# Kernel tuning notes

Measured on AMD Instinct MI355X. Metric: run time of the kernel, lower is better.

## Reference

```python
import jax, jax.numpy as jnp
import numpy as np
from jax import lax

B, C, D, H, W = 2, 128, 16, 16, 16
CH = C // 2
BN_EPS = 1e-5


def setup_inputs() -> dict:
    key = jax.random.key(0)
    ks = jax.random.split(key, 20)
    s = 0.02  # weight init scale
    inp = {
        "mri_feat": jax.random.normal(ks[0], (B, C, D, H, W), jnp.float32),
        "pet_feat": jax.random.normal(ks[1], (B, C, D, H, W), jnp.float32),
        # 1x1x1 conv projections stored as [out, in]
        "qw": jax.random.normal(ks[2], (C, C), jnp.float32) * s,
        "qb": jnp.zeros((C,), jnp.float32),
        "kw": jax.random.normal(ks[3], (C, C), jnp.float32) * s,
        "kb": jnp.zeros((C,), jnp.float32),
        "vw": jax.random.normal(ks[4], (C, C), jnp.float32) * s,
        "vb": jnp.zeros((C,), jnp.float32),
        # SE channel attention: C -> C/2 -> C
        "ca_w1": jax.random.normal(ks[5], (CH, C), jnp.float32) * s,
        "ca_b1": jnp.zeros((CH,), jnp.float32),
        "ca_w2": jax.random.normal(ks[6], (C, CH), jnp.float32) * s,
        "ca_b2": jnp.zeros((C,), jnp.float32),
        # conv1: 3x3x3 conv C -> C/2, then BN, then 1x1x1 conv C/2 -> C
        "c1_w": jax.random.normal(ks[7], (CH, C, 3, 3, 3), jnp.float32) * s,
        "c1_b": jnp.zeros((CH,), jnp.float32),
        "bn_gamma": jnp.ones((CH,), jnp.float32),
        "bn_beta": jnp.zeros((CH,), jnp.float32),
        "bn_mean": jnp.zeros((CH,), jnp.float32),
        "bn_var": jnp.ones((CH,), jnp.float32),
        "c2_w": jax.random.normal(ks[8], (C, CH), jnp.float32) * s,
        "c2_b": jnp.zeros((C,), jnp.float32),
    }
    return inp


def _conv1x1(x, w, b):
    # pointwise 3D conv == channel matmul
    return jnp.einsum('bcdhw,oc->bodhw', x, w) + b[None, :, None, None, None]


def reference(mri_feat, pet_feat, qw, qb, kw, kb, vw, vb,
              ca_w1, ca_b1, ca_w2, ca_b2,
              c1_w, c1_b, bn_gamma, bn_beta, bn_mean, bn_var,
              c2_w, c2_b):
    # --- SE channel attention on mri+pet ---
    pooled = jnp.mean(mri_feat + pet_feat, axis=(2, 3, 4))            # [B, C]
    t = jax.nn.relu(jnp.einsum('bc,oc->bo', pooled, ca_w1) + ca_b1)   # [B, C/2]
    cw = jax.nn.sigmoid(jnp.einsum('bh,oh->bo', t, ca_w2) + ca_b2)    # [B, C]
    cw = cw[:, :, None, None, None]
    mri_w = mri_feat * cw
    pet_w = pet_feat * cw

    # --- QKV (1x1x1 convs) ---
    Q = _conv1x1(mri_w, qw, qb)
    K = _conv1x1(pet_w, kw, kb)
    V = _conv1x1(pet_w, vw, vb)

    # --- full spatial cross attention ---
    scores = jnp.einsum('bcdhw,bcDHW->bdhwDHW', Q, K)   # [B,D,H,W,D,H,W]
    # NOTE: faithful to torch: softmax over LAST axis only (key W axis)
    attn = jax.nn.softmax(scores, axis=-1)
    fused = jnp.einsum('bdhwDHW,bcDHW->bcdhw', attn, V)

    # --- conv1 block: Conv3x3 -> ReLU -> BN(eval) -> Conv1x1 ---
    x = fused + mri_w
    y = lax.conv_general_dilated(
        x, c1_w, window_strides=(1, 1, 1), padding=((1, 1), (1, 1), (1, 1)),
        dimension_numbers=('NCDHW', 'OIDHW', 'NCDHW'))
    y = y + c1_b[None, :, None, None, None]
    y = jax.nn.relu(y)
    inv = lax.rsqrt(bn_var + BN_EPS)
    y = (y - bn_mean[None, :, None, None, None]) * (bn_gamma * inv)[None, :, None, None, None] \
        + bn_beta[None, :, None, None, None]
    out = _conv1x1(y, c2_w, c2_b)
    return out
```

## Files before the change

kernel.cpp:

```cpp
#include <hip/hip_runtime.h>
#include <hip/hip_bf16.h>
#include <math.h>

#define BB 2
#define CC 128
#define CHH 64
#define DD 16
#define NN 4096
#define SP 256
#define KTOT 3456
#define NKS 8

typedef float  f32x4 __attribute__((ext_vector_type(4)));
typedef short  s16x4 __attribute__((ext_vector_type(4)));
typedef short  s16x8 __attribute__((ext_vector_type(8)));

static __device__ __forceinline__ unsigned short f2bf(float x) {
    __hip_bfloat16 h = __float2bfloat16(x);
    return __builtin_bit_cast(unsigned short, h);
}

__global__ __launch_bounds__(256) void k_prep(const float* __restrict__ c1w, const float* __restrict__ c2w,
                                              const float* __restrict__ bg, const float* __restrict__ bbeta,
                                              const float* __restrict__ bm, const float* __restrict__ bv,
                                              const float* __restrict__ c2b,
                                              const float* __restrict__ qw, const float* __restrict__ kw,
                                              const float* __restrict__ vw,
                                              unsigned short* __restrict__ Wb,
                                              unsigned short* __restrict__ w2p,
                                              float* __restrict__ b2p,
                                              unsigned short* __restrict__ qwb,
                                              unsigned short* __restrict__ kwb,
                                              unsigned short* __restrict__ vwb) {
    int idx = blockIdx.x * 256 + threadIdx.x;
    for (int e = idx; e < CHH * KTOT; e += gridDim.x * 256) {
        int h = e / KTOT, rem = e % KTOT, tap = rem >> 7, c = rem & 127;
        Wb[e] = f2bf(c1w[(h * CC + c) * 27 + tap]);
    }
    for (int e = idx; e < CC * CC; e += gridDim.x * 256) {
        qwb[e] = f2bf(qw[e]);
        kwb[e] = f2bf(kw[e]);
        vwb[e] = f2bf(vw[e]);
    }
    for (int e = idx; e < CC * CHH; e += gridDim.x * 256) {
        int h = e & 63;
        float iv = rsqrtf(bv[h] + 1e-5f);
        w2p[e] = f2bf(c2w[e] * bg[h] * iv);
    }
    if (idx < CC) {
        float s = c2b[idx];
        for (int h = 0; h < CHH; h++) {
            float iv = rsqrtf(bv[h] + 1e-5f);
            s += c2w[idx * CHH + h] * (bbeta[h] - bm[h] * bg[h] * iv);
        }
        b2p[idx] = s;
    }
}

__global__ __launch_bounds__(256) void k_pool(const float* __restrict__ mri,
                                              const float* __restrict__ pet,
                                              float* __restrict__ pooled) {
    int bc = blockIdx.x;
    const float* m = mri + (size_t)bc * NN;
    const float* p = pet + (size_t)bc * NN;
    float s = 0.f;
    for (int i = threadIdx.x; i < NN; i += 256) s += m[i] + p[i];
    __shared__ float red[256];
    red[threadIdx.x] = s;
    __syncthreads();
    for (int off = 128; off > 0; off >>= 1) {
        if (threadIdx.x < off) red[threadIdx.x] += red[threadIdx.x + off];
        __syncthreads();
    }
    if (threadIdx.x == 0) pooled[bc] = red[0] * (1.0f / NN);
}

__global__ __launch_bounds__(128) void k_cw(const float* __restrict__ pooled,
                                            const float* __restrict__ w1, const float* __restrict__ b1,
                                            const float* __restrict__ w2, const float* __restrict__ b2,
                                            float* __restrict__ cw) {
    __shared__ float pl[BB * CC];
    __shared__ float tl[BB * CHH];
    int t = threadIdx.x;
    pl[t] = pooled[t];
    pl[t + 128] = pooled[t + 128];
    __syncthreads();
    {
        int b = t >> 6, h = t & 63;
        float acc = b1[h];
        for (int c = 0; c < CC; c++) acc += pl[b * CC + c] * w1[h * CC + c];
        tl[b * CHH + h] = fmaxf(acc, 0.f);
    }
    __syncthreads();
    for (int b = 0; b < BB; b++) {
        float acc = b2[t];
        for (int h = 0; h < CHH; h++) acc += tl[b * CHH + h] * w2[t * CHH + h];
        cw[b * CC + t] = 1.f / (1.f + __expf(-acc));
    }
}

__global__ __launch_bounds__(256) void k_qkv(const float* __restrict__ mri, const float* __restrict__ pet,
                                             const float* __restrict__ cw,
                                             const unsigned short* __restrict__ qwb, const float* __restrict__ qb,
                                             const unsigned short* __restrict__ kwb, const float* __restrict__ kb,
                                             const unsigned short* __restrict__ vwb, const float* __restrict__ vb,
                                             unsigned short* __restrict__ Qt, unsigned short* __restrict__ Kt,
                                             unsigned short* __restrict__ Vc) {
    __shared__ unsigned short am[32][136];
    __shared__ unsigned short ap[32][136];
    int blk = blockIdx.x;
    int b = blk >> 7;
    int n0 = (blk & 127) * 32;
    int t = threadIdx.x;
    for (int e = t; e < 64 * 32; e += 256) {
        int c2 = (e >> 5) << 1, j = e & 31;
        float cw0 = cw[b * CC + c2], cw1 = cw[b * CC + c2 + 1];
        size_t g0 = (size_t)(b * CC + c2) * NN + n0 + j;
        unsigned int pm = (unsigned int)f2bf(mri[g0] * cw0) | ((unsigned int)f2bf(mri[g0 + NN] * cw1) << 16);
        unsigned int pp = (unsigned int)f2bf(pet[g0] * cw0) | ((unsigned int)f2bf(pet[g0 + NN] * cw1) << 16);
        *(unsigned int*)&am[j][c2] = pm;
        *(unsigned int*)&ap[j][c2] = pp;
    }
    __syncthreads();
    int wv = t >> 6, lane = t & 63;
    int lrow = lane & 15, lg = lane >> 4;
    int o0 = wv * 32;

    s16x8 bf[2][4];
    s16x8 wf[2][4];
    f32x4 acc[2][2];

#define QKV_MAT(WPTR, BIAS, ACT)                                                            \
    {                                                                                       \
        _Pragma("unroll")                                                                   \
        for (int nt = 0; nt < 2; nt++)                                                      \
            _Pragma("unroll")                                                               \
            for (int ks = 0; ks < 4; ks++)                                                  \
                bf[nt][ks] = *(const s16x8*)&ACT[nt * 16 + lrow][ks * 32 + lg * 8];         \
        _Pragma("unroll")                                                                   \
        for (int m = 0; m < 2; m++)                                                         \
            _Pragma("unroll")                                                               \
            for (int ks = 0; ks < 4; ks++)                                                  \
                wf[m][ks] = *(const s16x8*)&WPTR[(size_t)(o0 + m * 16 + lrow) * CC + ks * 32 + lg * 8]; \
        _Pragma("unroll")                                                                   \
        for (int m = 0; m < 2; m++) {                                                       \
            float b0 = BIAS[o0 + m * 16 + lg * 4 + 0];                                      \
            float b1 = BIAS[o0 + m * 16 + lg * 4 + 1];                                      \
            float b2v = BIAS[o0 + m * 16 + lg * 4 + 2];                                     \
            float b3 = BIAS[o0 + m * 16 + lg * 4 + 3];                                      \
            _Pragma("unroll")                                                               \
            for (int nt = 0; nt < 2; nt++) {                                                \
                acc[m][nt] = (f32x4){b0, b1, b2v, b3};                                      \
                _Pragma("unroll")                                                           \
                for (int ks = 0; ks < 4; ks++)                                              \
                    acc[m][nt] = __builtin_amdgcn_mfma_f32_16x16x32_bf16(wf[m][ks], bf[nt][ks], acc[m][nt], 0, 0, 0); \
            }                                                                               \
        }                                                                                   \
    }

    QKV_MAT(qwb, qb, am);
#pragma unroll
    for (int m = 0; m < 2; m++)
#pragma unroll
        for (int nt = 0; nt < 2; nt++) {
            s16x4 q4;
#pragma unroll
            for (int r = 0; r < 4; r++) q4[r] = (short)f2bf(acc[m][nt][r]);
            *(s16x4*)&Qt[((size_t)b * NN + n0 + nt * 16 + lrow) * CC + o0 + m * 16 + lg * 4] = q4;
        }
    QKV_MAT(kwb, kb, ap);
#pragma unroll
    for (int m = 0; m < 2; m++)
#pragma unroll
        for (int nt = 0; nt < 2; nt++) {
            s16x4 k4;
#pragma unroll
            for (int r = 0; r < 4; r++) k4[r] = (short)f2bf(acc[m][nt][r]);
            *(s16x4*)&Kt[((size_t)b * NN + n0 + nt * 16 + lrow) * CC + o0 + m * 16 + lg * 4] = k4;
        }
    QKV_MAT(vwb, vb, ap);
#pragma unroll
    for (int m = 0; m < 2; m++)
#pragma unroll
        for (int nt = 0; nt < 2; nt++)
#pragma unroll
            for (int r = 0; r < 4; r++)
                Vc[((size_t)b * CC + o0 + m * 16 + lg * 4 + r) * NN + n0 + nt * 16 + lrow] =
                    (unsigned short)f2bf(acc[m][nt][r]);
#undef QKV_MAT
}

#define QW 32
__global__ __launch_bounds__(512) void k_attn(const unsigned short* __restrict__ Qt,
                                              const unsigned short* __restrict__ Kt,
                                              const unsigned short* __restrict__ Vc,
                                              float* __restrict__ Opart) {
    __shared__ unsigned short Ks[2][32][136];
    __shared__ unsigned short Vs[2][128][40];
    int bid = blockIdx.x;
    int ks = bid & 7;
    int r = bid >> 3;
    int qc = r >> 1;
    int b = r & 1;
    int t = threadIdx.x;
    int wv = t >> 6;
    int lane = t & 63;
    int lrow = lane & 15;
    int lg = lane >> 4;
    int q0 = qc * 256 + wv * 32;

    const unsigned short* Qb = Qt + (size_t)b * NN * CC;
    const unsigned short* Kb = Kt + (size_t)b * NN * CC;
    const unsigned short* Vb = Vc + (size_t)b * CC * NN;

    int sj = t >> 4, sseg = t & 15;
    int svc = t >> 2, svg = t & 3;

#define STAGE(BUF, K0)                                                                     \
    {                                                                                      \
        *(s16x8*)&Ks[BUF][sj][sseg * 8] = *(const s16x8*)(Kb + (size_t)((K0) + sj) * CC + sseg * 8); \
        *(s16x8*)&Vs[BUF][svc][svg * 8] = *(const s16x8*)(Vb + (size_t)svc * NN + (K0) + svg * 8);   \
    }

    s16x8 qf[2][4];
#pragma unroll
    for (int qt = 0; qt < 2; qt++)
#pragma unroll
        for (int cc = 0; cc < 4; cc++)
            qf[qt][cc] = *(const s16x8*)(Qb + (size_t)(q0 + qt * 16 + lrow) * CC + cc * 32 + lg * 8);

    f32x4 acc[2][8];
#pragma unroll
    for (int qt = 0; qt < 2; qt++)
#pragma unroll
        for (int ct = 0; ct < 8; ct++) acc[qt][ct] = (f32x4){0.f, 0.f, 0.f, 0.f};

    int kbase = ks * 512;
    STAGE(0, kbase);
#pragma unroll 1
    for (int i = 0; i < 16; i++) {
        __syncthreads();
        if (i + 1 < 16) STAGE((i + 1) & 1, kbase + (i + 1) * 32);
        int cur = i & 1;
        f32x4 sc[2][2];
#pragma unroll
        for (int kt = 0; kt < 2; kt++) {
            s16x8 kf[4];
#pragma unroll
            for (int cc = 0; cc < 4; cc++)
                kf[cc] = *(const s16x8*)&Ks[cur][kt * 16 + lrow][cc * 32 + lg * 8];
#pragma unroll
            for (int qt = 0; qt < 2; qt++) {
                f32x4 a = (f32x4){0.f, 0.f, 0.f, 0.f};
#pragma unroll
                for (int cc = 0; cc < 4; cc++)
                    a = __builtin_amdgcn_mfma_f32_16x16x32_bf16(kf[cc], qf[qt][cc], a, 0, 0, 0);
                sc[qt][kt] = a;
            }
        }
        s16x8 pf[2];
#pragma unroll
        for (int qt = 0; qt < 2; qt++) {
#pragma unroll
            for (int kt = 0; kt < 2; kt++) {
                f32x4 s = sc[qt][kt];
                float m = fmaxf(fmaxf(s[0], s[1]), fmaxf(s[2], s[3]));
                m = fmaxf(m, __shfl_xor(m, 16));
                m = fmaxf(m, __shfl_xor(m, 32));
                float e0 = __expf(s[0] - m), e1 = __expf(s[1] - m);
                float e2 = __expf(s[2] - m), e3 = __expf(s[3] - m);
                float sum = e0 + e1 + e2 + e3;
                sum += __shfl_xor(sum, 16);
                sum += __shfl_xor(sum, 32);
                float inv = 1.0f / sum;
                pf[qt][kt * 4 + 0] = (short)f2bf(e0 * inv);
                pf[qt][kt * 4 + 1] = (short)f2bf(e1 * inv);
                pf[qt][kt * 4 + 2] = (short)f2bf(e2 * inv);
                pf[qt][kt * 4 + 3] = (short)f2bf(e3 * inv);
            }
        }
#pragma unroll
        for (int ct = 0; ct < 8; ct++) {
            s16x4 v0 = *(const s16x4*)&Vs[cur][ct * 16 + lrow][4 * lg];
            s16x4 v1 = *(const s16x4*)&Vs[cur][ct * 16 + lrow][16 + 4 * lg];
            s16x8 vf = (s16x8){v0[0], v0[1], v0[2], v0[3], v1[0], v1[1], v1[2], v1[3]};
            acc[0][ct] = __builtin_amdgcn_mfma_f32_16x16x32_bf16(vf, pf[0], acc[0][ct], 0, 0, 0);
            acc[1][ct] = __builtin_amdgcn_mfma_f32_16x16x32_bf16(vf, pf[1], acc[1][ct], 0, 0, 0);
        }
    }
#undef STAGE
    float* Op = Opart + ((size_t)(ks * BB + b) * NN) * CC;
#pragma unroll
    for (int qt = 0; qt < 2; qt++)
#pragma unroll
        for (int ct = 0; ct < 8; ct++)
            *(f32x4*)&Op[(size_t)(q0 + qt * 16 + lrow) * CC + ct * 16 + lg * 4] = acc[qt][ct];
}

__global__ __launch_bounds__(256) void k_comb(const float* __restrict__ Opart,
                                              const float* __restrict__ mri, const float* __restrict__ cw,
                                              unsigned short* __restrict__ Xb) {
    __shared__ float tl[128][33];
    __shared__ float cws[128];
    int bid = blockIdx.x;
    int b = bid >> 7, n0 = (bid & 127) * 32;
    int t = threadIdx.x;
    if (t < 128) cws[t] = cw[b * CC + t];
    {
        int c = t >> 1, half = t & 1;
        const float* src = mri + (size_t)(b * CC + c) * NN + n0 + half * 16;
#pragma unroll
        for (int j = 0; j < 4; j++) {
            f32x4 v = *(const f32x4*)(src + j * 4);
            tl[c][half * 16 + j * 4 + 0] = v[0];
            tl[c][half * 16 + j * 4 + 1] = v[1];
            tl[c][half * 16 + j * 4 + 2] = v[2];
            tl[c][half * 16 + j * 4 + 3] = v[3];
        }
    }
    __syncthreads();
    {
        int n = t >> 3, c0 = (t & 7) * 16;
        size_t rowoff = (size_t)(n0 + n) * CC + c0;
        s16x8 o0v, o1v;
#pragma unroll
        for (int ci = 0; ci < 4; ci++) {
            f32x4 s = (f32x4){0.f, 0.f, 0.f, 0.f};
#pragma unroll
            for (int ks = 0; ks < NKS; ks++) {
                f32x4 p = *(const f32x4*)&Opart[((size_t)(ks * BB + b) * NN) * CC + rowoff + ci * 4];
                s[0] += p[0]; s[1] += p[1]; s[2] += p[2]; s[3] += p[3];
            }
#pragma unroll
            for (int j = 0; j < 4; j++) {
                int c = c0 + ci * 4 + j;
                float v = s[j] + tl[c][n] * cws[c];
                if (ci < 2) o0v[ci * 4 + j] = (short)f2bf(v);
                else        o1v[(ci - 2) * 4 + j] = (short)f2bf(v);
            }
        }
        unsigned short* dst = Xb + ((size_t)b * NN + n0 + n) * CC + c0;
        *(s16x8*)dst = o0v;
        *(s16x8*)(dst + 8) = o1v;
    }
}

__global__ __launch_bounds__(512) void k_attn_fb(const unsigned short* __restrict__ Qt,
                                                 const unsigned short* __restrict__ Kt,
                                                 const unsigned short* __restrict__ Vc,
                                                 const float* __restrict__ mri, const float* __restrict__ cw,
                                                 unsigned short* __restrict__ Xb) {
    __shared__ float Op[8][16][68];
    int bid = blockIdx.x;
    int lid = (bid & 7) * 32 + (bid >> 3);
    int b = lid >> 7;
    int q0 = (lid & 127) * QW;
    int t = threadIdx.x;
    int wv = t >> 6;
    int lane = t & 63;
    int lrow = lane & 15;
    int lg = lane >> 4;

    const unsigned short* Qb = Qt + (size_t)b * NN * CC;
    const unsigned short* Kb = Kt + (size_t)b * NN * CC;
    const unsigned short* Vb = Vc + (size_t)b * CC * NN;

    s16x8 qf[2][4];
#pragma unroll
    for (int qt = 0; qt < 2; qt++)
#pragma unroll
        for (int cc = 0; cc < 4; cc++)
            qf[qt][cc] = *(const s16x8*)(Qb + (size_t)(q0 + qt * 16 + lrow) * CC + cc * 32 + lg * 8);

    f32x4 acc[2][8];
#pragma unroll
    for (int qt = 0; qt < 2; qt++)
#pragma unroll
        for (int ct = 0; ct < 8; ct++) acc[qt][ct] = (f32x4){0.f, 0.f, 0.f, 0.f};

    for (int kg = wv; kg < 128; kg += 8) {
        int k0 = kg * 32;
        f32x4 sc[2][2];
#pragma unroll
        for (int kt = 0; kt < 2; kt++) {
            s16x8 kf[4];
#pragma unroll
            for (int cc = 0; cc < 4; cc++)
                kf[cc] = *(const s16x8*)(Kb + (size_t)(k0 + kt * 16 + lrow) * CC + cc * 32 + lg * 8);
#pragma unroll
            for (int qt = 0; qt < 2; qt++) {
                f32x4 a = (f32x4){0.f, 0.f, 0.f, 0.f};
#pragma unroll
                for (int cc = 0; cc < 4; cc++)
                    a = __builtin_amdgcn_mfma_f32_16x16x32_bf16(kf[cc], qf[qt][cc], a, 0, 0, 0);
                sc[qt][kt] = a;
            }
        }
        s16x8 pf[2];
#pragma unroll
        for (int qt = 0; qt < 2; qt++) {
#pragma unroll
            for (int kt = 0; kt < 2; kt++) {
                f32x4 s = sc[qt][kt];
                float m = fmaxf(fmaxf(s[0], s[1]), fmaxf(s[2], s[3]));
                m = fmaxf(m, __shfl_xor(m, 16));
                m = fmaxf(m, __shfl_xor(m, 32));
                float e0 = __expf(s[0] - m), e1 = __expf(s[1] - m);
                float e2 = __expf(s[2] - m), e3 = __expf(s[3] - m);
                float sum = e0 + e1 + e2 + e3;
                sum += __shfl_xor(sum, 16);
                sum += __shfl_xor(sum, 32);
                float inv = 1.0f / sum;
                pf[qt][kt * 4 + 0] = (short)f2bf(e0 * inv);
                pf[qt][kt * 4 + 1] = (short)f2bf(e1 * inv);
                pf[qt][kt * 4 + 2] = (short)f2bf(e2 * inv);
                pf[qt][kt * 4 + 3] = (short)f2bf(e3 * inv);
            }
        }
#pragma unroll
        for (int ct = 0; ct < 8; ct++) {
            const unsigned short* vp = Vb + (size_t)(ct * 16 + lrow) * NN + k0 + 4 * lg;
            s16x4 v0 = *(const s16x4*)vp;
            s16x4 v1 = *(const s16x4*)(vp + 16);
            s16x8 vf = (s16x8){v0[0], v0[1], v0[2], v0[3], v1[0], v1[1], v1[2], v1[3]};
            acc[0][ct] = __builtin_amdgcn_mfma_f32_16x16x32_bf16(vf, pf[0], acc[0][ct], 0, 0, 0);
            acc[1][ct] = __builtin_amdgcn_mfma_f32_16x16x32_bf16(vf, pf[1], acc[1][ct], 0, 0, 0);
        }
    }
#pragma unroll
    for (int p = 0; p < 4; p++) {
        int qt = p >> 1, ch = p & 1;
#pragma unroll
        for (int ci = 0; ci < 4; ci++)
            *(f32x4*)&Op[wv][lrow][ci * 16 + lg * 4] = acc[qt][ch * 4 + ci];
        __syncthreads();
#pragma unroll
        for (int rep = 0; rep < 2; rep++) {
            int e = t + rep * 512;
            int cl = e & 63, q = e >> 6;
            int c = ch * 64 + cl;
            float s = 0.f;
#pragma unroll
            for (int w = 0; w < 8; w++) s += Op[w][q][cl];
            int n = q0 + qt * 16 + q;
            size_t gi = ((size_t)b * CC + c) * NN + n;
            Xb[((size_t)b * NN + n) * CC + c] = f2bf(s + mri[gi] * cw[b * CC + c]);
        }
        __syncthreads();
    }
}

__global__ __launch_bounds__(256) void k_conv3(const unsigned short* __restrict__ Xb,
                                               const unsigned short* __restrict__ Wb,
                                               const float* __restrict__ c1b,
                                               unsigned short* __restrict__ Yb) {
    int bid = blockIdx.x;
    int b = bid >> 8;
    int d = (bid >> 4) & 15;
    int h0 = ((bid >> 2) & 3) * 16;
    int hp = (bid & 3) * 4;
    int t = threadIdx.x;
    int wv = t >> 6;
    int himg = hp + wv;
    int lane = t & 63;
    int lrow = lane & 15, lg = lane >> 4;

    const unsigned short* Wrow = Wb + (size_t)(h0 + lrow) * KTOT + lg * 8;
    const unsigned short* Xbase = Xb + (size_t)b * NN * CC + lg * 8;
    const s16x8 z8 = (s16x8){0, 0, 0, 0, 0, 0, 0, 0};

    f32x4 acc = (f32x4){0.f, 0.f, 0.f, 0.f};
    for (int kd = 0; kd < 3; kd++) {
        int dd2 = d + kd - 1;
        if ((unsigned)dd2 >= 16u) continue;
        for (int kh = 0; kh < 3; kh++) {
            int hh2 = himg + kh - 1;
            if ((unsigned)hh2 >= 16u) continue;
#pragma unroll
            for (int kw = 0; kw < 3; kw++) {
                int ww2 = lrow + kw - 1;
                bool okw = (unsigned)ww2 < 16u;
                int tap = (kd * 3 + kh) * 3 + kw;
                const unsigned short* wtap = Wrow + tap * CC;
                const unsigned short* xpos = Xbase + (size_t)(dd2 * 256 + hh2 * 16 + ww2) * CC;
                s16x8 a0 = *(const s16x8*)(wtap);
                s16x8 a1 = *(const s16x8*)(wtap + 32);
                s16x8 a2 = *(const s16x8*)(wtap + 64);
                s16x8 a3 = *(const s16x8*)(wtap + 96);
                s16x8 b0 = okw ? *(const s16x8*)(xpos) : z8;
                s16x8 b1 = okw ? *(const s16x8*)(xpos + 32) : z8;
                s16x8 b2 = okw ? *(const s16x8*)(xpos + 64) : z8;
                s16x8 b3 = okw ? *(const s16x8*)(xpos + 96) : z8;
                acc = __builtin_amdgcn_mfma_f32_16x16x32_bf16(a0, b0, acc, 0, 0, 0);
                acc = __builtin_amdgcn_mfma_f32_16x16x32_bf16(a1, b1, acc, 0, 0, 0);
                acc = __builtin_amdgcn_mfma_f32_16x16x32_bf16(a2, b2, acc, 0, 0, 0);
                acc = __builtin_amdgcn_mfma_f32_16x16x32_bf16(a3, b3, acc, 0, 0, 0);
            }
        }
    }
    int hloc = h0 + lg * 4;
    int n = d * 256 + himg * 16 + lrow;
    s16x4 yv;
#pragma unroll
    for (int r = 0; r < 4; r++) {
        float y = fmaxf(acc[r] + c1b[hloc + r], 0.f);
        yv[r] = (short)f2bf(y);
    }
    *(s16x4*)&Yb[((size_t)b * NN + n) * CHH + hloc] = yv;
}

__global__ __launch_bounds__(256) void k_out(const unsigned short* __restrict__ Yb,
                                             const unsigned short* __restrict__ w2p,
                                             const float* __restrict__ b2p,
                                             float* __restrict__ out) {
    int bid = blockIdx.x;
    int b = bid >> 7, n0 = (bid & 127) * 32;
    int t = threadIdx.x;
    int wv = t >> 6, lane = t & 63;
    int lrow = lane & 15, lg = lane >> 4;
    int o0 = wv * 32;

    f32x4 acc[2][2];
#pragma unroll
    for (int m = 0; m < 2; m++)
#pragma unroll
        for (int nt = 0; nt < 2; nt++) acc[m][nt] = (f32x4){0.f, 0.f, 0.f, 0.f};

#pragma unroll
    for (int ks = 0; ks < 2; ks++) {
        s16x8 a0 = *(const s16x8*)&w2p[(o0 + lrow) * CHH + ks * 32 + lg * 8];
        s16x8 a1 = *(const s16x8*)&w2p[(o0 + 16 + lrow) * CHH + ks * 32 + lg * 8];
        s16x8 f0 = *(const s16x8*)&Yb[((size_t)b * NN + n0 + lrow) * CHH + ks * 32 + lg * 8];
        s16x8 f1 = *(const s16x8*)&Yb[((size_t)b * NN + n0 + 16 + lrow) * CHH + ks * 32 + lg * 8];
        acc[0][0] = __builtin_amdgcn_mfma_f32_16x16x32_bf16(a0, f0, acc[0][0], 0, 0, 0);
        acc[0][1] = __builtin_amdgcn_mfma_f32_16x16x32_bf16(a0, f1, acc[0][1], 0, 0, 0);
        acc[1][0] = __builtin_amdgcn_mfma_f32_16x16x32_bf16(a1, f0, acc[1][0], 0, 0, 0);
        acc[1][1] = __builtin_amdgcn_mfma_f32_16x16x32_bf16(a1, f1, acc[1][1], 0, 0, 0);
    }
#pragma unroll
    for (int m = 0; m < 2; m++) {
#pragma unroll
        for (int r = 0; r < 4; r++) {
            int o = o0 + m * 16 + lg * 4 + r;
            float bias = b2p[o];
#pragma unroll
            for (int nt = 0; nt < 2; nt++) {
                int n = n0 + nt * 16 + lrow;
                out[((size_t)b * CC + o) * NN + n] = acc[m][nt][r] + bias;
            }
        }
    }
}

extern "C" void kernel_launch(void* const* d_in, const int* in_sizes, int n_in,
                              void* d_out, int out_size, void* d_ws, size_t ws_size,
                              hipStream_t stream) {
    const float* mri = (const float*)d_in[0];
    const float* pet = (const float*)d_in[1];
    const float* qw  = (const float*)d_in[2];
    const float* qb  = (const float*)d_in[3];
    const float* kw  = (const float*)d_in[4];
    const float* kb  = (const float*)d_in[5];
    const float* vw  = (const float*)d_in[6];
    const float* vb  = (const float*)d_in[7];
    const float* w1  = (const float*)d_in[8];
    const float* b1  = (const float*)d_in[9];
    const float* w2  = (const float*)d_in[10];
    const float* b2  = (const float*)d_in[11];
    const float* c1w = (const float*)d_in[12];
    const float* c1b = (const float*)d_in[13];
    const float* bg  = (const float*)d_in[14];
    const float* bbeta = (const float*)d_in[15];
    const float* bm  = (const float*)d_in[16];
    const float* bv  = (const float*)d_in[17];
    const float* c2w = (const float*)d_in[18];
    const float* c2b = (const float*)d_in[19];
    float* out = (float*)d_out;

    float* ws = (float*)d_ws;
    float* pooled = ws;
    float* cwb    = ws + 256;
    float* b2p    = ws + 512;
    unsigned short* Qt  = (unsigned short*)(ws + 1024);
    unsigned short* Kt  = Qt + (size_t)BB * NN * CC;
    unsigned short* Vc  = Kt + (size_t)BB * NN * CC;
    unsigned short* Xb  = Vc + (size_t)BB * NN * CC;
    unsigned short* Yb  = Xb + (size_t)BB * NN * CC;
    unsigned short* Wb  = Yb + (size_t)BB * NN * CHH;
    unsigned short* w2p = Wb + (size_t)CHH * KTOT;
    unsigned short* qwb = w2p + (size_t)CC * CHH;
    unsigned short* kwb = qwb + (size_t)CC * CC;
    unsigned short* vwb = kwb + (size_t)CC * CC;
    size_t head_bytes = (size_t)((char*)(vwb + (size_t)CC * CC) - (char*)d_ws);
    head_bytes = (head_bytes + 15) & ~(size_t)15;
    float* Opart = (float*)((char*)d_ws + head_bytes);
    size_t opart_bytes = (size_t)NKS * BB * NN * CC * sizeof(float);
    bool use_split = (head_bytes + opart_bytes) <= ws_size;

    k_prep<<<64, 256, 0, stream>>>(c1w, c2w, bg, bbeta, bm, bv, c2b, qw, kw, vw,
                                   Wb, w2p, b2p, qwb, kwb, vwb);
    k_pool<<<BB * CC, 256, 0, stream>>>(mri, pet, pooled);
    k_cw<<<1, 128, 0, stream>>>(pooled, w1, b1, w2, b2, cwb);
    k_qkv<<<BB * (NN / 32), 256, 0, stream>>>(mri, pet, cwb, qwb, qb, kwb, kb, vwb, vb, Qt, Kt, Vc);
    if (use_split) {
        k_attn<<<256, 512, 0, stream>>>(Qt, Kt, Vc, Opart);
        k_comb<<<BB * (NN / 32), 256, 0, stream>>>(Opart, mri, cwb, Xb);
    } else {
        k_attn_fb<<<BB * (NN / QW), 512, 0, stream>>>(Qt, Kt, Vc, mri, cwb, Xb);
    }
    k_conv3<<<512, 256, 0, stream>>>(Xb, Wb, c1b, Yb);
    k_out<<<256, 256, 0, stream>>>(Yb, w2p, b2p, out);
}
```

Measured before the change: 137.6 us.

## Stage conv3 input halo and weights in LDS with double-buffered taps

Rewrites the 3x3x3 conv kernel so each block loads its input halo (3 depth x 4 height x 18 width x 128 channels) into shared memory once and streams the per-tap weight slice through a double-buffered LDS tile. Before, every wave fetched weights and inputs straight from global memory for each tap. Each block now covers all 64 output channels for two image rows with 8 waves, so the grid is half as large and each block twice as wide. In exchange it adds a barrier per tap and uses a large amount of shared memory, which may limit occupancy.

```diff
diff --git a/kernel.cpp b/kernel.cpp
--- a/kernel.cpp
+++ b/kernel.cpp
@@ -450,63 +450,79 @@
     }
 }
 
-__global__ __launch_bounds__(256) void k_conv3(const unsigned short* __restrict__ Xb,
+__global__ __launch_bounds__(512) void k_conv3(const unsigned short* __restrict__ Xb,
                                                const unsigned short* __restrict__ Wb,
                                                const float* __restrict__ c1b,
                                                unsigned short* __restrict__ Yb) {
+    __shared__ unsigned short Xs[3][4][18][136];
+    __shared__ unsigned short Ws[2][64][136];
     int bid = blockIdx.x;
-    int b = bid >> 8;
-    int d = (bid >> 4) & 15;
-    int h0 = ((bid >> 2) & 3) * 16;
-    int hp = (bid & 3) * 4;
+    int b = bid >> 7;
+    int d = (bid >> 3) & 15;
+    int hp = (bid & 7) * 2;
     int t = threadIdx.x;
     int wv = t >> 6;
-    int himg = hp + wv;
     int lane = t & 63;
     int lrow = lane & 15, lg = lane >> 4;
-
-    const unsigned short* Wrow = Wb + (size_t)(h0 + lrow) * KTOT + lg * 8;
-    const unsigned short* Xbase = Xb + (size_t)b * NN * CC + lg * 8;
-    const s16x8 z8 = (s16x8){0, 0, 0, 0, 0, 0, 0, 0};
+    int mt = wv >> 1;
+    int nt = wv & 1;
+
+    const unsigned short* Xbase = Xb + (size_t)b * NN * CC;
+
+    {
+        unsigned short* xz = &Xs[0][0][0][0];
+        const s16x8 z8 = (s16x8){0, 0, 0, 0, 0, 0, 0, 0};
+        for (int e = t; e < (3 * 4 * 18 * 136) / 8; e += 512)
+            *(s16x8*)(xz + e * 8) = z8;
+    }
+    __syncthreads();
+    for (int e = t; e < 3 * 4 * 16 * 16; e += 512) {
+        int seg = e & 15;
+        int w = (e >> 4) & 15;
+        int sh = (e >> 8) & 3;
+        int sd = e >> 10;
+        int dd2 = d - 1 + sd, hh2 = hp - 1 + sh;
+        if ((unsigned)dd2 < 16u && (unsigned)hh2 < 16u) {
+            int n = dd2 * 256 + hh2 * 16 + w;
+            *(s16x8*)&Xs[sd][sh][w + 1][seg * 8] = *(const s16x8*)(Xbase + (size_t)n * CC + seg * 8);
+        }
+    }
+
+#define WSTAGE(BUF, TAP)                                                       \
+    for (int e = t; e < 1024; e += 512) {                                      \
+        int row = e >> 4, seg = e & 15;                                        \
+        *(s16x8*)&Ws[BUF][row][seg * 8] =                                      \
+            *(const s16x8*)(Wb + (size_t)row * KTOT + (TAP) * 128 + seg * 8);  \
+    }
+    WSTAGE(0, 0);
 
     f32x4 acc = (f32x4){0.f, 0.f, 0.f, 0.f};
-    for (int kd = 0; kd < 3; kd++) {
-        int dd2 = d + kd - 1;
-        if ((unsigned)dd2 >= 16u) continue;
-        for (int kh = 0; kh < 3; kh++) {
-            int hh2 = himg + kh - 1;
-            if ((unsigned)hh2 >= 16u) continue;
-#pragma unroll
-            for (int kw = 0; kw < 3; kw++) {
-                int ww2 = lrow + kw - 1;
-                bool okw = (unsigned)ww2 < 16u;
-                int tap = (kd * 3 + kh) * 3 + kw;
-                const unsigned short* wtap = Wrow + tap * CC;
-                const unsigned short* xpos = Xbase + (size_t)(dd2 * 256 + hh2 * 16 + ww2) * CC;
-                s16x8 a0 = *(const s16x8*)(wtap);
-                s16x8 a1 = *(const s16x8*)(wtap + 32);
-                s16x8 a2 = *(const s16x8*)(wtap + 64);
-                s16x8 a3 = *(const s16x8*)(wtap + 96);
-                s16x8 b0 = okw ? *(const s16x8*)(xpos) : z8;
-                s16x8 b1 = okw ? *(const s16x8*)(xpos + 32) : z8;
-                s16x8 b2 = okw ? *(const s16x8*)(xpos + 64) : z8;
-                s16x8 b3 = okw ? *(const s16x8*)(xpos + 96) : z8;
-                acc = __builtin_amdgcn_mfma_f32_16x16x32_bf16(a0, b0, acc, 0, 0, 0);
-                acc = __builtin_amdgcn_mfma_f32_16x16x32_bf16(a1, b1, acc, 0, 0, 0);
-                acc = __builtin_amdgcn_mfma_f32_16x16x32_bf16(a2, b2, acc, 0, 0, 0);
-                acc = __builtin_amdgcn_mfma_f32_16x16x32_bf16(a3, b3, acc, 0, 0, 0);
-            }
-        }
-    }
-    int hloc = h0 + lg * 4;
-    int n = d * 256 + himg * 16 + lrow;
+#pragma unroll 1
+    for (int tap = 0; tap < 27; tap++) {
+        __syncthreads();
+        if (tap + 1 < 27) { WSTAGE((tap + 1) & 1, tap + 1); }
+        int cur = tap & 1;
+        int kd = tap / 9;
+        int rem = tap - kd * 9;
+        int kh = rem / 3;
+        int kw = rem - kh * 3;
+#pragma unroll
+        for (int cc = 0; cc < 4; cc++) {
+            s16x8 af = *(const s16x8*)&Ws[cur][mt * 16 + lrow][cc * 32 + lg * 8];
+            s16x8 bfv = *(const s16x8*)&Xs[kd][nt + kh][lrow + kw][cc * 32 + lg * 8];
+            acc = __builtin_amdgcn_mfma_f32_16x16x32_bf16(af, bfv, acc, 0, 0, 0);
+        }
+    }
+#undef WSTAGE
+    int ch0 = mt * 16 + lg * 4;
+    int n = d * 256 + (hp + nt) * 16 + lrow;
     s16x4 yv;
 #pragma unroll
     for (int r = 0; r < 4; r++) {
-        float y = fmaxf(acc[r] + c1b[hloc + r], 0.f);
+        float y = fmaxf(acc[r] + c1b[ch0 + r], 0.f);
         yv[r] = (short)f2bf(y);
     }
-    *(s16x4*)&Yb[((size_t)b * NN + n) * CHH + hloc] = yv;
+    *(s16x4*)&Yb[((size_t)b * NN + n) * CHH + ch0] = yv;
 }
 
 __global__ __launch_bounds__(256) void k_out(const unsigned short* __restrict__ Yb,
@@ -608,6 +624,6 @@
     } else {
         k_attn_fb<<<BB * (NN / QW), 512, 0, stream>>>(Qt, Kt, Vc, mri, cwb, Xb);
     }
-    k_conv3<<<512, 256, 0, stream>>>(Xb, Wb, c1b, Yb);
+    k_conv3<<<256, 512, 0, stream>>>(Xb, Wb, c1b, Yb);
     k_out<<<256, 256, 0, stream>>>(Yb, w2p, b2p, out);
 }
```

After: 120.2 us. -12.7%, faster.
